# Optimization experiments

Hardware: AMD Instinct MI355X
Metric: run time of the kernel (lower is better)

Reference implementation:

```python
import jax, jax.numpy as jnp
import numpy as np
from math import sqrt


def setup_inputs() -> dict:
    key = jax.random.key(0)
    ks = jax.random.split(key, 5)
    B, S, D = 4, 2048, 1024
    scale = 0.02
    return {
        "x": jax.random.normal(ks[0], (B, S, D), dtype=jnp.float32),
        "Wq": jax.random.normal(ks[1], (D, D), dtype=jnp.float32) * scale,
        "Wk": jax.random.normal(ks[2], (D, D), dtype=jnp.float32) * scale,
        "Wv": jax.random.normal(ks[3], (D, D), dtype=jnp.float32) * scale,
        "Wo": jax.random.normal(ks[4], (D, D), dtype=jnp.float32) * scale,
    }


def reference(x, Wq, Wk, Wv, Wo):
    NUM_HEAD = 16
    B, S, D = x.shape
    d_k = D // NUM_HEAD

    # fused QKV projection: weights are (d_model, d_in), applied as W @ x^T -> x @ W^T
    q = jnp.einsum('od,bsd->bso', Wq, x)
    k = jnp.einsum('od,bsd->bso', Wk, x)
    v = jnp.einsum('od,bsd->bso', Wv, x)

    def split_heads(t):  # [B,S,D] -> [B,H,S,d_k]
        return t.reshape(B, S, NUM_HEAD, d_k).transpose(0, 2, 1, 3)

    q, k, v = split_heads(q), split_heads(k), split_heads(v)

    # naive causal attention: full [B,H,S,S] score matrix
    scores = jnp.einsum('bhqd,bhkd->bhqk', q, k) / sqrt(d_k)
    causal = jnp.tril(jnp.ones((S, S), dtype=bool))  # [S,S]
    scores = jnp.where(causal, scores, -jnp.inf)
    probs = jax.nn.softmax(scores, axis=-1)
    attn = jnp.einsum('bhqk,bhkd->bhqd', probs, v)

    # merge heads: [B,H,S,d_k] -> [B,S,D]
    attn = attn.transpose(0, 2, 1, 3).reshape(B, S, D)
    # output projection
    return jnp.einsum('om,bsm->bso', Wo, attn)
```

## Files before the change

### kernel.cpp

```cpp
#include <hip/hip_runtime.h>
#include <hip/hip_bf16.h>
#include <stdint.h>

typedef unsigned short u16;
typedef __attribute__((ext_vector_type(8))) short bf16x8;
typedef __attribute__((ext_vector_type(4))) float f32x4;
typedef __attribute__((ext_vector_type(16))) float f32x16;

#define AS1 __attribute__((address_space(1)))
#define AS3 __attribute__((address_space(3)))

__device__ __forceinline__ u16 f2bf(float f) {
  union { float f; uint32_t u; } v; v.f = f;
  uint32_t u = v.u;
  return (u16)((u + 0x7FFFu + ((u >> 16) & 1u)) >> 16);
}

__device__ __forceinline__ uint32_t cvtpk(float lo, float hi) {
  uint32_t d;
  asm("v_cvt_pk_bf16_f32 %0, %1, %2" : "=v"(d) : "v"(lo), "v"(hi));
  return d;
}

__global__ __launch_bounds__(256) void cvt_all_kernel(const float* __restrict__ x,
    const float* __restrict__ Wq, const float* __restrict__ Wk,
    const float* __restrict__ Wv, const float* __restrict__ Wo,
    u16* __restrict__ xb, u16* __restrict__ wqb, u16* __restrict__ wkb,
    u16* __restrict__ wvb, u16* __restrict__ wob) {
  const int bid = blockIdx.x;
  const float* s;
  u16* d;
  int i;
  if (bid < 8192) {
    s = x; d = xb; i = bid * 256 + threadIdx.x;
  } else {
    const int w = (bid - 8192) >> 10;
    i = ((bid - 8192) & 1023) * 256 + threadIdx.x;
    s = (w == 0) ? Wq : (w == 1) ? Wk : (w == 2) ? Wv : Wo;
    d = (w == 0) ? wqb : (w == 1) ? wkb : (w == 2) ? wvb : wob;
  }
  float4 v = reinterpret_cast<const float4*>(s)[i];
  uint2 o;
  o.x = cvtpk(v.x, v.y);
  o.y = cvtpk(v.z, v.w);
  reinterpret_cast<uint2*>(d)[i] = o;
}

#define QSCALE 0.18033688011112042f

#define GK 64

template <int MODE, int KC, typename OutT>
__device__ __forceinline__ void gemm128_body(u16* __restrict__ lds,
    const u16* __restrict__ A, const u16* __restrict__ Bm, OutT* __restrict__ C,
    int M, int N, int by, int bx, float oscale) {
  const int tid = threadIdx.x;
  const int lane = tid & 63;
  const int wave = tid >> 6;
  const int wm = wave >> 1, wn = wave & 1;
  const int l15 = lane & 15, lhi = lane >> 4;
  const int axor = (lane & 7) << 4;

  const int srow = tid >> 3;
  const int scol = (((tid & 7) ^ (srow & 7)) << 4);
  const size_t Kb = (size_t)KC * 2;
  const uint8_t* Ag = (const uint8_t*)A + (size_t)(by * 128 + srow) * Kb + scol;
  const uint8_t* Bg = (const uint8_t*)Bm + (size_t)(bx * 128 + srow) * Kb + scol;
  uint8_t* Lb = (uint8_t*)lds;

#define STG128(bufi, kt)                                                                  \
  do {                                                                                    \
    _Pragma("unroll") for (int c = 0; c < 4; ++c) {                                       \
      __builtin_amdgcn_global_load_lds(                                                   \
          (const AS1 uint32_t*)(Ag + (size_t)c * 32 * Kb + (size_t)(kt) * 128),           \
          (AS3 uint32_t*)(Lb + (bufi) * 32768 + c * 4096 + tid * 16), 16, 0, 0);          \
      __builtin_amdgcn_global_load_lds(                                                   \
          (const AS1 uint32_t*)(Bg + (size_t)c * 32 * Kb + (size_t)(kt) * 128),           \
          (AS3 uint32_t*)(Lb + (bufi) * 32768 + 16384 + c * 4096 + tid * 16), 16, 0, 0);  \
    }                                                                                     \
  } while (0)

  const f32x4 fzero = {0.f, 0.f, 0.f, 0.f};
  f32x4 acc[4][4];
#pragma unroll
  for (int m = 0; m < 4; ++m)
#pragma unroll
    for (int n = 0; n < 4; ++n) acc[m][n] = fzero;

  constexpr int NT = KC / GK;

  STG128(0, 0);
  __syncthreads();

#pragma unroll
  for (int t = 0; t < NT; ++t) {
    const int cur = t & 1;
    if (t + 1 < NT) STG128(cur ^ 1, t + 1);
    const uint8_t* Ab = Lb + cur * 32768;
    const uint8_t* Bb = Ab + 16384;
    bf16x8 aF[4][2], bF[4][2];
#pragma unroll
    for (int ff = 0; ff < 4; ++ff)
#pragma unroll
      for (int ks = 0; ks < 2; ++ks) {
        aF[ff][ks] = *reinterpret_cast<const bf16x8*>(
            Ab + (wm * 64 + ff * 16 + l15) * 128 + ((ks * 64 + lhi * 16) ^ axor));
        bF[ff][ks] = *reinterpret_cast<const bf16x8*>(
            Bb + (wn * 64 + ff * 16 + l15) * 128 + ((ks * 64 + lhi * 16) ^ axor));
      }
    __builtin_amdgcn_s_setprio(1);
#pragma unroll
    for (int mm = 0; mm < 4; ++mm)
#pragma unroll
      for (int nn = 0; nn < 4; ++nn)
#pragma unroll
        for (int ks = 0; ks < 2; ++ks)
          acc[mm][nn] = __builtin_amdgcn_mfma_f32_16x16x32_bf16(aF[mm][ks], bF[nn][ks],
                                                                acc[mm][nn], 0, 0, 0);
    __builtin_amdgcn_s_setprio(0);
    __syncthreads();
  }

#pragma unroll
  for (int mf = 0; mf < 4; ++mf)
#pragma unroll
    for (int nf = 0; nf < 4; ++nf) {
      const int row0 = by * 128 + wm * 64 + mf * 16 + lhi * 4;
      const int col = bx * 128 + wn * 64 + nf * 16 + l15;
      if constexpr (MODE == 2) {
        uint2 pk;
        pk.x = cvtpk(acc[mf][nf][0], acc[mf][nf][1]);
        pk.y = cvtpk(acc[mf][nf][2], acc[mf][nf][3]);
        *reinterpret_cast<uint2*>((u16*)C + (size_t)col * M + row0) = pk;
      } else if constexpr (MODE == 1) {
#pragma unroll
        for (int r = 0; r < 4; ++r)
          ((float*)C)[(size_t)(row0 + r) * N + col] = acc[mf][nf][r];
      } else {
#pragma unroll
        for (int r = 0; r < 4; ++r)
          ((u16*)C)[(size_t)(row0 + r) * N + col] = f2bf(acc[mf][nf][r] * oscale);
      }
    }
#undef STG128
}

__global__ __launch_bounds__(256, 2) void gemm_qkv_kernel(const u16* __restrict__ A,
    const u16* __restrict__ W0, const u16* __restrict__ W1, const u16* __restrict__ W2,
    u16* __restrict__ OQ, u16* __restrict__ OK, u16* __restrict__ OVT, int M, int N) {
  __shared__ u16 lds[2][2][128 * GK];
  const int id = blockIdx.x;
  const int xcd = id & 7;
  const int slot = id >> 3;
  const int bz = slot >> 6;
  const int r = slot & 63;
  const int byi = r >> 3, bx = r & 7;
  const int by = xcd + 8 * byi;
  if (bz == 0)      gemm128_body<0, 1024, u16>(&lds[0][0][0], A, W0, OQ,  M, N, by, bx, QSCALE);
  else if (bz == 1) gemm128_body<0, 1024, u16>(&lds[0][0][0], A, W1, OK,  M, N, by, bx, 1.f);
  else              gemm128_body<2, 1024, u16>(&lds[0][0][0], A, W2, OVT, M, N, by, bx, 1.f);
}

__global__ __launch_bounds__(256, 2) void gemm_out_kernel(const u16* __restrict__ A,
    const u16* __restrict__ Bm, float* __restrict__ C, int M, int N) {
  __shared__ u16 lds[2][2][128 * GK];
  const int id = blockIdx.x;
  const int xcd = id & 7;
  const int slot = id >> 3;
  const int byi = slot >> 3, bx = slot & 7;
  const int by = xcd + 8 * byi;
  gemm128_body<1, 1024, float>(&lds[0][0][0], A, Bm, C, M, N, by, bx, 1.f);
}

#define KVB 64

__global__ __launch_bounds__(512, 4) void attn_kernel(const u16* __restrict__ Q,
    const u16* __restrict__ Kg, const u16* __restrict__ VTg, u16* __restrict__ O,
    int S, int H, int Dm, int T) {
  const int bh = blockIdx.x;
  const int b = bh / H, h = bh % H;
  const int by = blockIdx.y;
  const int y = (by < 4) ? (7 - by) : (by - 4);
  const int qH = 1024 + y * 128;
  const int qL = 896 - y * 128;
  const int tid = threadIdx.x;
  const int lane = tid & 63, wave = tid >> 6;
  const int l31 = lane & 31, hi = lane >> 5;

  __shared__ u16 KVs[2][2][64 * 64];

  const u16* Qh = Q + ((size_t)b * S) * Dm + h * 64;
  const u16* Kh = Kg + ((size_t)b * S) * Dm + h * 64;
  const u16* Vh = VTg + (size_t)(h * 64) * T + (size_t)b * S;
  const int qv = (wave < 4) ? (qH + wave * 32) : (qL + (wave - 4) * 32);
  const int qr = qv + l31;

  bf16x8 qf[4];
#pragma unroll
  for (int dc = 0; dc < 4; ++dc)
    qf[dc] = *reinterpret_cast<const bf16x8*>(Qh + (size_t)qr * Dm + dc * 16 + hi * 8);

  f32x16 acc[2];
#pragma unroll
  for (int db = 0; db < 2; ++db)
#pragma unroll
    for (int r = 0; r < 16; ++r) acc[db][r] = 0.f;
  float mrow = -1e30f, lrow = 0.f;

#define STAGE(bufi, kvoff)                                                                     \
  do {                                                                                         \
    const int srow = tid >> 3;                                                                 \
    const int scol = (((tid & 7) ^ (srow & 7)) << 3);                                          \
    __builtin_amdgcn_global_load_lds(                                                          \
        (const AS1 uint32_t*)(Kh + (size_t)((kvoff) + srow) * Dm + scol),                      \
        (AS3 uint32_t*)(&KVs[bufi][0][tid * 8]), 16, 0, 0);                                    \
    __builtin_amdgcn_global_load_lds(                                                          \
        (const AS1 uint32_t*)(Vh + (size_t)srow * T + (kvoff) + scol),                         \
        (AS3 uint32_t*)(&KVs[bufi][1][tid * 8]), 16, 0, 0);                                    \
  } while (0)

  const int nt = qH / 64 + 2;
  STAGE(0, 0);
  int buf = 0;

  for (int t = 0; t < nt; ++t) {
    __syncthreads();
    const int kv = t * KVB;
    if (t + 1 < nt) STAGE(buf ^ 1, (t + 1) * KVB);

    if (kv <= qv + 31) {
      const u16* KB = KVs[buf][0];
      const u16* VB = KVs[buf][1];

      f32x16 sc[2];
#pragma unroll
      for (int bb = 0; bb < 2; ++bb) {
#pragma unroll
        for (int r = 0; r < 16; ++r) sc[bb][r] = 0.f;
#pragma unroll
        for (int dc = 0; dc < 4; ++dc) {
          const bf16x8 kf = *reinterpret_cast<const bf16x8*>(
              KB + (bb * 32 + l31) * 64 + (((dc * 2 + hi) ^ (l31 & 7)) << 3));
          sc[bb] = __builtin_amdgcn_mfma_f32_32x32x16_bf16(kf, qf[dc], sc[bb], 0, 0, 0);
        }
      }

      const bool msk = (kv + KVB - 1 > qv);
      float bmax = -3e38f;
#pragma unroll
      for (int bb = 0; bb < 2; ++bb)
#pragma unroll
        for (int r = 0; r < 16; ++r) {
          float v = sc[bb][r];
          if (msk) {
            const int kvg = kv + bb * 32 + (r & 3) + 8 * (r >> 2) + 4 * hi;
            v = (kvg > qr) ? -1e30f : v;
            sc[bb][r] = v;
          }
          bmax = fmaxf(bmax, v);
        }
      bmax = fmaxf(bmax, __shfl_xor(bmax, 32, 64));

      if (!__all(bmax <= mrow + 6.f)) {
        const float mn = fmaxf(mrow, bmax);
        const float fac = __builtin_amdgcn_exp2f(mrow - mn);
        mrow = mn;
        lrow *= fac;
#pragma unroll
        for (int db = 0; db < 2; ++db)
#pragma unroll
          for (int r = 0; r < 16; ++r) acc[db][r] *= fac;
      }

      float rs = 0.f;
#pragma unroll
      for (int bb = 0; bb < 2; ++bb)
#pragma unroll
        for (int r = 0; r < 16; ++r) {
          const float p = __builtin_amdgcn_exp2f(sc[bb][r] - mrow);
          sc[bb][r] = p;
          rs += p;
        }
      lrow += rs;

#pragma unroll
      for (int cc = 0; cc < 4; ++cc) {
        const int bb = cc >> 1, c2 = cc & 1;
        uint32_t a0 = cvtpk(sc[bb][8 * c2 + 0], sc[bb][8 * c2 + 1]);
        uint32_t a1 = cvtpk(sc[bb][8 * c2 + 2], sc[bb][8 * c2 + 3]);
        uint32_t b0 = cvtpk(sc[bb][8 * c2 + 4], sc[bb][8 * c2 + 5]);
        uint32_t b1 = cvtpk(sc[bb][8 * c2 + 6], sc[bb][8 * c2 + 7]);
        asm("v_permlane32_swap_b32 %0, %1" : "+v"(a0), "+v"(b0));
        asm("v_permlane32_swap_b32 %0, %1" : "+v"(a1), "+v"(b1));
        union { uint32_t u[4]; bf16x8 v8; } pf;
        pf.u[0] = a0; pf.u[1] = a1; pf.u[2] = b0; pf.u[3] = b1;
#pragma unroll
        for (int db = 0; db < 2; ++db) {
          const bf16x8 vfg = *reinterpret_cast<const bf16x8*>(
              VB + (db * 32 + l31) * 64 + (((cc * 2 + hi) ^ (l31 & 7)) << 3));
          acc[db] = __builtin_amdgcn_mfma_f32_32x32x16_bf16(vfg, pf.v8, acc[db], 0, 0, 0);
        }
      }
    }
    buf ^= 1;
  }

  lrow += __shfl_xor(lrow, 32, 64);
  const float inv = 1.f / lrow;
  __syncthreads();
  u16* Ost = &KVs[0][0][0];
  {
    const int row = wave * 32 + l31;
#pragma unroll
    for (int db = 0; db < 2; ++db)
#pragma unroll
      for (int g = 0; g < 4; ++g) {
        uint2 pk;
        pk.x = cvtpk(acc[db][4 * g + 0] * inv, acc[db][4 * g + 1] * inv);
        pk.y = cvtpk(acc[db][4 * g + 2] * inv, acc[db][4 * g + 3] * inv);
        const int blk = 4 * db + g;
        const int addr = row * 64 + (((blk ^ (row & 7)) << 3)) + 4 * hi;
        *reinterpret_cast<uint2*>(Ost + addr) = pk;
      }
  }
  __syncthreads();
#pragma unroll
  for (int p = 0; p < 4; ++p) {
    const int idx = p * 512 + tid;
    const int row = idx >> 3, seg = idx & 7;
    const float4 v = *reinterpret_cast<const float4*>(Ost + row * 64 + ((seg ^ (row & 7)) << 3));
    const int q = (row < 128) ? (qH + row) : (qL + row - 128);
    *reinterpret_cast<float4*>(O + ((size_t)b * S + q) * Dm + h * 64 + seg * 8) = v;
  }
#undef STAGE
}

extern "C" void kernel_launch(void* const* d_in, const int* in_sizes, int n_in,
                              void* d_out, int out_size, void* d_ws, size_t ws_size,
                              hipStream_t stream) {
  const float* x  = (const float*)d_in[0];
  const float* Wq = (const float*)d_in[1];
  const float* Wk = (const float*)d_in[2];
  const float* Wv = (const float*)d_in[3];
  const float* Wo = (const float*)d_in[4];
  float* out = (float*)d_out;

  const int B = 4, S = 2048, D = 1024, H = 16;
  const int T = B * S;

  uint8_t* p = (uint8_t*)d_ws;
  u16* xb  = (u16*)p; p += (size_t)T * D * 2;
  u16* wqb = (u16*)p; p += (size_t)D * D * 2;
  u16* wkb = (u16*)p; p += (size_t)D * D * 2;
  u16* wvb = (u16*)p; p += (size_t)D * D * 2;
  u16* wob = (u16*)p; p += (size_t)D * D * 2;
  u16* Qb  = (u16*)p; p += (size_t)T * D * 2;
  u16* Kb  = (u16*)p; p += (size_t)T * D * 2;
  u16* VTb = (u16*)p; p += (size_t)D * T * 2;
  u16* Ab  = xb;

  cvt_all_kernel<<<dim3(12288), dim3(256), 0, stream>>>(x, Wq, Wk, Wv, Wo,
                                                        xb, wqb, wkb, wvb, wob);

  gemm_qkv_kernel<<<dim3(1536), dim3(256), 0, stream>>>(xb, wqb, wkb, wvb, Qb, Kb, VTb, T, D);

  attn_kernel<<<dim3(B * H, 8), dim3(512), 0, stream>>>(Qb, Kb, VTb, Ab, S, H, D, T);

  gemm_out_kernel<<<dim3(512), dim3(256), 0, stream>>>(Ab, wob, out, T, D);
}
```

Baseline: 145.7 us.

## Process two query strips per wave in attention to halve block threads

The attention kernel now uses 256 threads per block. Each wave owns two 32-row query strips, a high one and a low one, paired so causal work balances, and runs the shared K/V tile against both strips. Each LDS K/V tile is therefore reused twice per wave, and each thread issues two staging loads per tile. The cost is roughly double the register state per wave (two sets of accumulators and Q fragments) and a drop in launch bounds from 4 to 2 waves per SIMD, which could hurt latency hiding.

```diff
diff --git a/kernel.cpp b/kernel.cpp
--- a/kernel.cpp
+++ b/kernel.cpp
@@ -174,52 +174,129 @@
 
 #define KVB 64
 
-__global__ __launch_bounds__(512, 4) void attn_kernel(const u16* __restrict__ Q,
+__device__ __forceinline__ void attn_tile(const u16* __restrict__ KB,
+    const u16* __restrict__ VB, const bf16x8 (&qf)[4], f32x16 (&acc)[2],
+    float& mrow, float& lrow, int kv, int qv, int qr, int l31, int lh) {
+  f32x16 sc[2];
+#pragma unroll
+  for (int bb = 0; bb < 2; ++bb) {
+#pragma unroll
+    for (int r = 0; r < 16; ++r) sc[bb][r] = 0.f;
+#pragma unroll
+    for (int dc = 0; dc < 4; ++dc) {
+      const bf16x8 kf = *reinterpret_cast<const bf16x8*>(
+          KB + (bb * 32 + l31) * 64 + (((dc * 2 + lh) ^ (l31 & 7)) << 3));
+      sc[bb] = __builtin_amdgcn_mfma_f32_32x32x16_bf16(kf, qf[dc], sc[bb], 0, 0, 0);
+    }
+  }
+
+  const bool msk = (kv + KVB - 1 > qv);
+  float bmax = -3e38f;
+#pragma unroll
+  for (int bb = 0; bb < 2; ++bb)
+#pragma unroll
+    for (int r = 0; r < 16; ++r) {
+      float v = sc[bb][r];
+      if (msk) {
+        const int kvg = kv + bb * 32 + (r & 3) + 8 * (r >> 2) + 4 * lh;
+        v = (kvg > qr) ? -1e30f : v;
+        sc[bb][r] = v;
+      }
+      bmax = fmaxf(bmax, v);
+    }
+  bmax = fmaxf(bmax, __shfl_xor(bmax, 32, 64));
+
+  if (!__all(bmax <= mrow + 6.f)) {
+    const float mn = fmaxf(mrow, bmax);
+    const float fac = __builtin_amdgcn_exp2f(mrow - mn);
+    mrow = mn;
+    lrow *= fac;
+#pragma unroll
+    for (int db = 0; db < 2; ++db)
+#pragma unroll
+      for (int r = 0; r < 16; ++r) acc[db][r] *= fac;
+  }
+
+  float rs = 0.f;
+#pragma unroll
+  for (int bb = 0; bb < 2; ++bb)
+#pragma unroll
+    for (int r = 0; r < 16; ++r) {
+      const float p = __builtin_amdgcn_exp2f(sc[bb][r] - mrow);
+      sc[bb][r] = p;
+      rs += p;
+    }
+  lrow += rs;
+
+#pragma unroll
+  for (int cc = 0; cc < 4; ++cc) {
+    const int bb = cc >> 1, c2 = cc & 1;
+    uint32_t a0 = cvtpk(sc[bb][8 * c2 + 0], sc[bb][8 * c2 + 1]);
+    uint32_t a1 = cvtpk(sc[bb][8 * c2 + 2], sc[bb][8 * c2 + 3]);
+    uint32_t b0 = cvtpk(sc[bb][8 * c2 + 4], sc[bb][8 * c2 + 5]);
+    uint32_t b1 = cvtpk(sc[bb][8 * c2 + 6], sc[bb][8 * c2 + 7]);
+    asm("v_permlane32_swap_b32 %0, %1" : "+v"(a0), "+v"(b0));
+    asm("v_permlane32_swap_b32 %0, %1" : "+v"(a1), "+v"(b1));
+    union { uint32_t u[4]; bf16x8 v8; } pf;
+    pf.u[0] = a0; pf.u[1] = a1; pf.u[2] = b0; pf.u[3] = b1;
+#pragma unroll
+    for (int db = 0; db < 2; ++db) {
+      const bf16x8 vfg = *reinterpret_cast<const bf16x8*>(
+          VB + (db * 32 + l31) * 64 + (((cc * 2 + lh) ^ (l31 & 7)) << 3));
+      acc[db] = __builtin_amdgcn_mfma_f32_32x32x16_bf16(vfg, pf.v8, acc[db], 0, 0, 0);
+    }
+  }
+}
+
+__global__ __launch_bounds__(256, 2) void attn_kernel(const u16* __restrict__ Q,
     const u16* __restrict__ Kg, const u16* __restrict__ VTg, u16* __restrict__ O,
     int S, int H, int Dm, int T) {
   const int bh = blockIdx.x;
   const int b = bh / H, h = bh % H;
-  const int by = blockIdx.y;
-  const int y = (by < 4) ? (7 - by) : (by - 4);
-  const int qH = 1024 + y * 128;
-  const int qL = 896 - y * 128;
+  const int y = blockIdx.y;
+  const int qh0 = 1920 - 128 * y;
+  const int ql0 = 128 * y;
   const int tid = threadIdx.x;
   const int lane = tid & 63, wave = tid >> 6;
-  const int l31 = lane & 31, hi = lane >> 5;
+  const int l31 = lane & 31, lh = lane >> 5;
 
   __shared__ u16 KVs[2][2][64 * 64];
 
   const u16* Qh = Q + ((size_t)b * S) * Dm + h * 64;
   const u16* Kh = Kg + ((size_t)b * S) * Dm + h * 64;
   const u16* Vh = VTg + (size_t)(h * 64) * T + (size_t)b * S;
-  const int qv = (wave < 4) ? (qH + wave * 32) : (qL + (wave - 4) * 32);
-  const int qr = qv + l31;
-
-  bf16x8 qf[4];
-#pragma unroll
-  for (int dc = 0; dc < 4; ++dc)
-    qf[dc] = *reinterpret_cast<const bf16x8*>(Qh + (size_t)qr * Dm + dc * 16 + hi * 8);
-
-  f32x16 acc[2];
+  const int qvH = qh0 + wave * 32, qvL = ql0 + wave * 32;
+  const int qrH = qvH + l31, qrL = qvL + l31;
+
+  bf16x8 qfH[4], qfL[4];
+#pragma unroll
+  for (int dc = 0; dc < 4; ++dc) {
+    qfH[dc] = *reinterpret_cast<const bf16x8*>(Qh + (size_t)qrH * Dm + dc * 16 + lh * 8);
+    qfL[dc] = *reinterpret_cast<const bf16x8*>(Qh + (size_t)qrL * Dm + dc * 16 + lh * 8);
+  }
+
+  f32x16 accH[2], accL[2];
 #pragma unroll
   for (int db = 0; db < 2; ++db)
 #pragma unroll
-    for (int r = 0; r < 16; ++r) acc[db][r] = 0.f;
-  float mrow = -1e30f, lrow = 0.f;
+    for (int r = 0; r < 16; ++r) { accH[db][r] = 0.f; accL[db][r] = 0.f; }
+  float mH = -1e30f, lH = 0.f, mL = -1e30f, lL = 0.f;
 
 #define STAGE(bufi, kvoff)                                                                     \
   do {                                                                                         \
-    const int srow = tid >> 3;                                                                 \
-    const int scol = (((tid & 7) ^ (srow & 7)) << 3);                                          \
-    __builtin_amdgcn_global_load_lds(                                                          \
-        (const AS1 uint32_t*)(Kh + (size_t)((kvoff) + srow) * Dm + scol),                      \
-        (AS3 uint32_t*)(&KVs[bufi][0][tid * 8]), 16, 0, 0);                                    \
-    __builtin_amdgcn_global_load_lds(                                                          \
-        (const AS1 uint32_t*)(Vh + (size_t)srow * T + (kvoff) + scol),                         \
-        (AS3 uint32_t*)(&KVs[bufi][1][tid * 8]), 16, 0, 0);                                    \
+    const int sr = tid >> 3;                                                                   \
+    const int sc_ = (((tid & 7) ^ (sr & 7)) << 3);                                             \
+    _Pragma("unroll") for (int j = 0; j < 2; ++j) {                                            \
+      __builtin_amdgcn_global_load_lds(                                                        \
+          (const AS1 uint32_t*)(Kh + (size_t)((kvoff) + j * 32 + sr) * Dm + sc_),              \
+          (AS3 uint32_t*)(&KVs[bufi][0][j * 2048 + tid * 8]), 16, 0, 0);                       \
+      __builtin_amdgcn_global_load_lds(                                                        \
+          (const AS1 uint32_t*)(Vh + (size_t)(j * 32 + sr) * T + (kvoff) + sc_),               \
+          (AS3 uint32_t*)(&KVs[bufi][1][j * 2048 + tid * 8]), 16, 0, 0);                       \
+    }                                                                                          \
   } while (0)
 
-  const int nt = qH / 64 + 2;
+  const int nt = (qh0 + 128) / 64;
   STAGE(0, 0);
   int buf = 0;
 
@@ -227,109 +304,44 @@
     __syncthreads();
     const int kv = t * KVB;
     if (t + 1 < nt) STAGE(buf ^ 1, (t + 1) * KVB);
-
-    if (kv <= qv + 31) {
-      const u16* KB = KVs[buf][0];
-      const u16* VB = KVs[buf][1];
-
-      f32x16 sc[2];
-#pragma unroll
-      for (int bb = 0; bb < 2; ++bb) {
-#pragma unroll
-        for (int r = 0; r < 16; ++r) sc[bb][r] = 0.f;
-#pragma unroll
-        for (int dc = 0; dc < 4; ++dc) {
-          const bf16x8 kf = *reinterpret_cast<const bf16x8*>(
-              KB + (bb * 32 + l31) * 64 + (((dc * 2 + hi) ^ (l31 & 7)) << 3));
-          sc[bb] = __builtin_amdgcn_mfma_f32_32x32x16_bf16(kf, qf[dc], sc[bb], 0, 0, 0);
-        }
-      }
-
-      const bool msk = (kv + KVB - 1 > qv);
-      float bmax = -3e38f;
-#pragma unroll
-      for (int bb = 0; bb < 2; ++bb)
-#pragma unroll
-        for (int r = 0; r < 16; ++r) {
-          float v = sc[bb][r];
-          if (msk) {
-            const int kvg = kv + bb * 32 + (r & 3) + 8 * (r >> 2) + 4 * hi;
-            v = (kvg > qr) ? -1e30f : v;
-            sc[bb][r] = v;
-          }
-          bmax = fmaxf(bmax, v);
-        }
-      bmax = fmaxf(bmax, __shfl_xor(bmax, 32, 64));
-
-      if (!__all(bmax <= mrow + 6.f)) {
-        const float mn = fmaxf(mrow, bmax);
-        const float fac = __builtin_amdgcn_exp2f(mrow - mn);
-        mrow = mn;
-        lrow *= fac;
-#pragma unroll
-        for (int db = 0; db < 2; ++db)
-#pragma unroll
-          for (int r = 0; r < 16; ++r) acc[db][r] *= fac;
-      }
-
-      float rs = 0.f;
-#pragma unroll
-      for (int bb = 0; bb < 2; ++bb)
-#pragma unroll
-        for (int r = 0; r < 16; ++r) {
-          const float p = __builtin_amdgcn_exp2f(sc[bb][r] - mrow);
-          sc[bb][r] = p;
-          rs += p;
-        }
-      lrow += rs;
-
-#pragma unroll
-      for (int cc = 0; cc < 4; ++cc) {
-        const int bb = cc >> 1, c2 = cc & 1;
-        uint32_t a0 = cvtpk(sc[bb][8 * c2 + 0], sc[bb][8 * c2 + 1]);
-        uint32_t a1 = cvtpk(sc[bb][8 * c2 + 2], sc[bb][8 * c2 + 3]);
-        uint32_t b0 = cvtpk(sc[bb][8 * c2 + 4], sc[bb][8 * c2 + 5]);
-        uint32_t b1 = cvtpk(sc[bb][8 * c2 + 6], sc[bb][8 * c2 + 7]);
-        asm("v_permlane32_swap_b32 %0, %1" : "+v"(a0), "+v"(b0));
-        asm("v_permlane32_swap_b32 %0, %1" : "+v"(a1), "+v"(b1));
-        union { uint32_t u[4]; bf16x8 v8; } pf;
-        pf.u[0] = a0; pf.u[1] = a1; pf.u[2] = b0; pf.u[3] = b1;
-#pragma unroll
-        for (int db = 0; db < 2; ++db) {
-          const bf16x8 vfg = *reinterpret_cast<const bf16x8*>(
-              VB + (db * 32 + l31) * 64 + (((cc * 2 + hi) ^ (l31 & 7)) << 3));
-          acc[db] = __builtin_amdgcn_mfma_f32_32x32x16_bf16(vfg, pf.v8, acc[db], 0, 0, 0);
-        }
-      }
-    }
+    const u16* KB = KVs[buf][0];
+    const u16* VB = KVs[buf][1];
+    if (kv <= qvH + 31) attn_tile(KB, VB, qfH, accH, mH, lH, kv, qvH, qrH, l31, lh);
+    if (kv <= qvL + 31) attn_tile(KB, VB, qfL, accL, mL, lL, kv, qvL, qrL, l31, lh);
     buf ^= 1;
   }
 
-  lrow += __shfl_xor(lrow, 32, 64);
-  const float inv = 1.f / lrow;
+  lH += __shfl_xor(lH, 32, 64);
+  lL += __shfl_xor(lL, 32, 64);
+  const float invH = 1.f / lH, invL = 1.f / lL;
   __syncthreads();
   u16* Ost = &KVs[0][0][0];
   {
-    const int row = wave * 32 + l31;
-#pragma unroll
-    for (int db = 0; db < 2; ++db)
-#pragma unroll
-      for (int g = 0; g < 4; ++g) {
-        uint2 pk;
-        pk.x = cvtpk(acc[db][4 * g + 0] * inv, acc[db][4 * g + 1] * inv);
-        pk.y = cvtpk(acc[db][4 * g + 2] * inv, acc[db][4 * g + 3] * inv);
-        const int blk = 4 * db + g;
-        const int addr = row * 64 + (((blk ^ (row & 7)) << 3)) + 4 * hi;
-        *reinterpret_cast<uint2*>(Ost + addr) = pk;
-      }
+#pragma unroll
+    for (int s = 0; s < 2; ++s) {
+      const int row = s * 128 + wave * 32 + l31;
+      const f32x16* ac = s ? accL : accH;
+      const float inv = s ? invL : invH;
+#pragma unroll
+      for (int db = 0; db < 2; ++db)
+#pragma unroll
+        for (int g = 0; g < 4; ++g) {
+          uint2 pk;
+          pk.x = cvtpk(ac[db][4 * g + 0] * inv, ac[db][4 * g + 1] * inv);
+          pk.y = cvtpk(ac[db][4 * g + 2] * inv, ac[db][4 * g + 3] * inv);
+          const int blk = 4 * db + g;
+          const int addr = row * 64 + (((blk ^ (row & 7)) << 3)) + 4 * lh;
+          *reinterpret_cast<uint2*>(Ost + addr) = pk;
+        }
+    }
   }
   __syncthreads();
 #pragma unroll
-  for (int p = 0; p < 4; ++p) {
-    const int idx = p * 512 + tid;
+  for (int p = 0; p < 8; ++p) {
+    const int idx = p * 256 + tid;
     const int row = idx >> 3, seg = idx & 7;
     const float4 v = *reinterpret_cast<const float4*>(Ost + row * 64 + ((seg ^ (row & 7)) << 3));
-    const int q = (row < 128) ? (qH + row) : (qL + row - 128);
+    const int q = (row < 128) ? (qh0 + row) : (ql0 + row - 128);
     *reinterpret_cast<float4*>(O + ((size_t)b * S + q) * Dm + h * 64 + seg * 8) = v;
   }
 #undef STAGE
@@ -364,7 +376,7 @@
 
   gemm_qkv_kernel<<<dim3(1536), dim3(256), 0, stream>>>(xb, wqb, wkb, wvb, Qb, Kb, VTb, T, D);
 
-  attn_kernel<<<dim3(B * H, 8), dim3(512), 0, stream>>>(Qb, Kb, VTb, Ab, S, H, D, T);
+  attn_kernel<<<dim3(B * H, 8), dim3(256), 0, stream>>>(Qb, Kb, VTb, Ab, S, H, D, T);
 
   gemm_out_kernel<<<dim3(512), dim3(256), 0, stream>>>(Ab, wob, out, T, D);
 }
```

After: 145.3 us. No clear change (-0.3%).
